# Performance work log

Measured on AMD Instinct MI355X. Metric: run time of the kernel, lower is better.

Reference implementation:

```python
import jax, jax.numpy as jnp
import numpy as np

B, T, D, H = 1, 2048, 1024, 16
HD = D // H
STRIDE = T // 256  # hierarchical global stride (T > 512 branch)


def _mha(q_in, k_in, v_in, Wqkv, bqkv, Wo, bo, nh):
    """torch nn.MultiheadAttention (batch_first, eval/no-dropout), returns (out, head-avg attn)."""
    b, tq, d = q_in.shape
    hd = d // nh
    Wq, Wk, Wv = jnp.split(Wqkv, 3, axis=0)
    bq, bk, bv = jnp.split(bqkv, 3)
    def heads(x, W, bb):
        return (x @ W.T + bb).reshape(b, x.shape[1], nh, hd).transpose(0, 2, 1, 3)
    q = heads(q_in, Wq, bq)
    k = heads(k_in, Wk, bk)
    v = heads(v_in, Wv, bv)
    scores = jnp.einsum('bhtd,bhsd->bhts', q, k) / np.float32(np.sqrt(hd))
    attn = jax.nn.softmax(scores, axis=-1)
    out = jnp.einsum('bhts,bhsd->bhtd', attn, v).transpose(0, 2, 1, 3).reshape(b, tq, d)
    return out @ Wo.T + bo, attn.mean(axis=1)


def _interp_linear(x, size):
    """F.interpolate(mode='linear', align_corners=False) along axis 1. x: [B, Ts, C]."""
    ts = x.shape[1]
    src = (jnp.arange(size, dtype=x.dtype) + 0.5) * (ts / size) - 0.5
    src = jnp.clip(src, 0.0, ts - 1)
    i0 = jnp.floor(src).astype(jnp.int32)
    i1 = jnp.minimum(i0 + 1, ts - 1)
    w = (src - i0.astype(x.dtype))[None, :, None]
    return x[:, i0, :] * (1.0 - w) + x[:, i1, :] * w


def setup_inputs() -> dict:
    rng = jax.random.key(0)
    ks = iter(jax.random.split(rng, 32))
    s = 0.02
    n = lambda shape: jax.random.normal(next(ks), shape, dtype=jnp.float32) * s
    return {
        'query': jax.random.normal(next(ks), (B, T, D), jnp.float32),
        'key': jax.random.normal(next(ks), (B, T, D), jnp.float32),
        'value': jax.random.normal(next(ks), (B, T, D), jnp.float32),
        'strategy_probs': jax.nn.softmax(jax.random.normal(next(ks), (B, 4), jnp.float32), -1),
        'Wqkv_lin': n((3 * D, D)), 'b_lin': jnp.zeros((3 * D,), jnp.float32),
        'Wo_lin': n((D, D)), 'bo_lin': jnp.zeros((D,), jnp.float32),
        'sparsity_pattern': jax.random.normal(next(ks), (H, 1, 1), jnp.float32),
        'Wqkv_loc': n((3 * D, D)), 'b_loc': jnp.zeros((3 * D,), jnp.float32),
        'Wo_loc': n((D, D)), 'bo_loc': jnp.zeros((D,), jnp.float32),
        'Wqkv_glb': n((3 * D, D)), 'b_glb': jnp.zeros((3 * D,), jnp.float32),
        'Wo_glb': n((D, D)), 'bo_glb': jnp.zeros((D,), jnp.float32),
        'Wf': n((D, 2 * D)), 'bf': jnp.zeros((D,), jnp.float32),
        'R_quant': jax.random.normal(next(ks), (H, HD, HD), jnp.float32),
        'ent_gate': jax.random.normal(next(ks), (H, 2, 2), jnp.float32),
    }


def reference(query, key, value, strategy_probs, Wqkv_lin, b_lin, Wo_lin, bo_lin,
              sparsity_pattern, Wqkv_loc, b_loc, Wo_loc, bo_loc,
              Wqkv_glb, b_glb, Wo_glb, bo_glb, Wf, bf, R_quant, ent_gate):
    b, t, d = query.shape
    hd = d // H
    scale = np.float32(np.sqrt(hd))
    # --- 1) "linear" branch: standard MHA ---
    linear_out, linear_w = _mha(query, key, value, Wqkv_lin, b_lin, Wo_lin, bo_lin, H)
    # --- 2) sparse branch (per-head learned on/off mask on raw scores) ---
    qh = query.reshape(b, t, H, hd).transpose(0, 2, 1, 3)
    kh = key.reshape(b, t, H, hd).transpose(0, 2, 1, 3)
    vh = value.reshape(b, t, H, hd).transpose(0, 2, 1, 3)
    scores = jnp.einsum('bhtd,bhsd->bhts', qh, kh) / scale
    mask = (jax.nn.sigmoid(sparsity_pattern) > 0.5).astype(scores.dtype)  # [H,1,1]
    sp_attn = jax.nn.softmax(scores * mask[None], axis=-1)
    sparse_out = jnp.einsum('bhts,bhsd->bhtd', sp_attn, vh).transpose(0, 2, 1, 3).reshape(b, t, d)
    sparse_w = sp_attn.mean(axis=1)
    # --- 3) hierarchical branch (T > 512 path: strided global + linear interp) ---
    local_out, _ = _mha(query, key, value, Wqkv_loc, b_loc, Wo_loc, bo_loc, H // 2)
    gq, gk, gv = query[:, ::STRIDE], key[:, ::STRIDE], value[:, ::STRIDE]
    g_small, _ = _mha(gq, gk, gv, Wqkv_glb, b_glb, Wo_glb, bo_glb, H // 2)
    global_out = _interp_linear(g_small, t)
    hier_out = jnp.concatenate([local_out, global_out], axis=-1) @ Wf.T + bf
    # --- 4) quantum branch (per-head rotation + scalar gate on scores) ---
    q_rot = jnp.einsum('bhtd,hde->bhte', qh, R_quant)
    k_rot = jnp.einsum('bhtd,hde->bhte', kh, R_quant)
    gate = jax.nn.sigmoid(ent_gate[:, 0, 0])[None, :, None, None]  # [1,H,1,1]
    q_attn = jax.nn.softmax((jnp.einsum('bhtd,bhsd->bhts', q_rot, k_rot) / scale) * gate, axis=-1)
    quantum_out = jnp.einsum('bhts,bhsd->bhtd', q_attn, vh).transpose(0, 2, 1, 3).reshape(b, t, d)
    quantum_w = q_attn.mean(axis=1)
    # --- blend via strategy probabilities ---
    sp = strategy_probs[:, :, None]  # [B,4,1]
    all_out = jnp.stack([linear_out, sparse_out, hier_out, quantum_out], axis=1)  # [B,4,T,D]
    weighted = (all_out * sp[..., None]).sum(axis=1)  # [B,T,D]
    wstack = jnp.stack([linear_w, sparse_w, quantum_w], axis=1)  # [B,3,T,T]
    wsel = sp[:, jnp.array([0, 1, 3])][..., None, None]  # [B,3,1,1,1] (faithful to source; requires B==1)
    combined = (wstack * wsel).sum(axis=1)
    return weighted, combined
```

## Files before the change

kernel.cpp:

```cpp
#include <hip/hip_runtime.h>
#include <math.h>

#define D_MODEL 1024

typedef __attribute__((ext_vector_type(8))) short bf16x8;
typedef __attribute__((ext_vector_type(4))) float f32x4;
typedef __attribute__((ext_vector_type(8))) unsigned short u16x8;

__device__ __forceinline__ unsigned short bfr(float f) {
    unsigned u = __float_as_uint(f);
    u += 0x7fffu + ((u >> 16) & 1u);
    return (unsigned short)(u >> 16);
}
__device__ __forceinline__ float bff(unsigned short s) {
    return __uint_as_float(((unsigned)s) << 16);
}
__device__ __forceinline__ void split2(float x, unsigned short &h, unsigned short &l) {
    h = bfr(x);
    l = bfr(x - bff(h));
}
__device__ __forceinline__ unsigned cvtpk(float a, float b) {
    unsigned r;
    asm("v_cvt_pk_bf16_f32 %0, %1, %2" : "=v"(r) : "v"(a), "v"(b));
    return r;
}
__device__ __forceinline__ f32x4 mfma3(bf16x8 ah, bf16x8 al, bf16x8 bh, bf16x8 bl, f32x4 c) {
    c = __builtin_amdgcn_mfma_f32_16x16x32_bf16(ah, bh, c, 0, 0, 0);
    c = __builtin_amdgcn_mfma_f32_16x16x32_bf16(ah, bl, c, 0, 0, 0);
    c = __builtin_amdgcn_mfma_f32_16x16x32_bf16(al, bh, c, 0, 0, 0);
    return c;
}

__global__ __launch_bounds__(256) void split_rm(
    const float* __restrict__ in, unsigned short* __restrict__ hi,
    unsigned short* __restrict__ lo, int n4)
{
    int idx = blockIdx.x * 256 + threadIdx.x;
    if (idx >= n4) return;
    float4 v = ((const float4*)in)[idx];
    ushort4 hs, ls;
    split2(v.x, hs.x, ls.x); split2(v.y, hs.y, ls.y);
    split2(v.z, hs.z, ls.z); split2(v.w, hs.w, ls.w);
    ((ushort4*)hi)[idx] = hs;
    ((ushort4*)lo)[idx] = ls;
}

__global__ __launch_bounds__(256) void split_tr(
    const float* __restrict__ in, unsigned short* __restrict__ hi,
    unsigned short* __restrict__ lo, int T)
{
    __shared__ float xs[64][65];
    const int t0 = blockIdx.x * 64, d0 = blockIdx.y * 64;
    for (int idx = threadIdx.x; idx < 64 * 16; idx += 256) {
        int r = idx >> 4, c4 = (idx & 15) * 4;
        float4 v = *(const float4*)&in[(size_t)(t0 + r) * D_MODEL + d0 + c4];
        xs[r][c4] = v.x; xs[r][c4 + 1] = v.y; xs[r][c4 + 2] = v.z; xs[r][c4 + 3] = v.w;
    }
    __syncthreads();
    for (int idx = threadIdx.x; idx < 64 * 8; idx += 256) {
        int dd = idx >> 3, t8 = (idx & 7) * 8;
        u16x8 hs, ls;
#pragma unroll
        for (int j = 0; j < 8; ++j) {
            unsigned short hh, ll;
            split2(xs[t8 + j][dd], hh, ll);
            hs[j] = hh; ls[j] = ll;
        }
        *(u16x8*)&hi[(size_t)(d0 + dd) * T + t0 + t8] = hs;
        *(u16x8*)&lo[(size_t)(d0 + dd) * T + t0 + t8] = ls;
    }
}

__global__ __launch_bounds__(256) void gemm_mfma(
    const float* __restrict__ X, int xrstride,
    const float* __restrict__ W, int wrstride,
    const float* __restrict__ bias,
    float* __restrict__ C, int M, int N, int K,
    const float* __restrict__ sptr, int sidx, int accum)
{
    __shared__ unsigned short Xh[64][40], Xl[64][40];
    __shared__ unsigned short Wh[64][40], Wl[64][40];
    const int tid = threadIdx.x;
    const int m0 = blockIdx.x * 64, n0 = blockIdx.y * 64;
    const int lane = tid & 63, wave = tid >> 6;
    const int c = lane & 15, quad = lane >> 4;
    const int mbase = wave * 16;

    f32x4 acc[4];
#pragma unroll
    for (int nt = 0; nt < 4; ++nt) acc[nt] = (f32x4){0.f, 0.f, 0.f, 0.f};

    float4 xr[2], wr[2];
    const int r_ = tid >> 3, d4_ = (tid & 7) * 4;
    const int r2_ = (tid + 256) >> 3, d42_ = ((tid + 256) & 7) * 4;
    auto ldXW = [&](int k0) {
        xr[0] = *(const float4*)&X[(size_t)(m0 + r_) * xrstride + k0 + d4_];
        xr[1] = *(const float4*)&X[(size_t)(m0 + r2_) * xrstride + k0 + d42_];
        wr[0] = *(const float4*)&W[(size_t)(n0 + r_) * wrstride + k0 + d4_];
        wr[1] = *(const float4*)&W[(size_t)(n0 + r2_) * wrstride + k0 + d42_];
    };
    ldXW(0);

    for (int k0 = 0; k0 < K; k0 += 32) {
        __syncthreads();
        {
            ushort4 hs, ls;
            split2(xr[0].x, hs.x, ls.x); split2(xr[0].y, hs.y, ls.y);
            split2(xr[0].z, hs.z, ls.z); split2(xr[0].w, hs.w, ls.w);
            *(ushort4*)&Xh[r_][d4_] = hs; *(ushort4*)&Xl[r_][d4_] = ls;
            split2(xr[1].x, hs.x, ls.x); split2(xr[1].y, hs.y, ls.y);
            split2(xr[1].z, hs.z, ls.z); split2(xr[1].w, hs.w, ls.w);
            *(ushort4*)&Xh[r2_][d42_] = hs; *(ushort4*)&Xl[r2_][d42_] = ls;
            split2(wr[0].x, hs.x, ls.x); split2(wr[0].y, hs.y, ls.y);
            split2(wr[0].z, hs.z, ls.z); split2(wr[0].w, hs.w, ls.w);
            *(ushort4*)&Wh[r_][d4_] = hs; *(ushort4*)&Wl[r_][d4_] = ls;
            split2(wr[1].x, hs.x, ls.x); split2(wr[1].y, hs.y, ls.y);
            split2(wr[1].z, hs.z, ls.z); split2(wr[1].w, hs.w, ls.w);
            *(ushort4*)&Wh[r2_][d42_] = hs; *(ushort4*)&Wl[r2_][d42_] = ls;
        }
        __syncthreads();
        if (k0 + 32 < K) ldXW(k0 + 32);
        bf16x8 ah = *(const bf16x8*)&Xh[mbase + c][quad * 8];
        bf16x8 al = *(const bf16x8*)&Xl[mbase + c][quad * 8];
#pragma unroll
        for (int nt = 0; nt < 4; ++nt) {
            bf16x8 bh = *(const bf16x8*)&Wh[nt * 16 + c][quad * 8];
            bf16x8 bl = *(const bf16x8*)&Wl[nt * 16 + c][quad * 8];
            acc[nt] = mfma3(ah, al, bh, bl, acc[nt]);
        }
    }
    const float s = (sptr != nullptr) ? sptr[sidx] : 1.0f;
#pragma unroll
    for (int nt = 0; nt < 4; ++nt) {
#pragma unroll
        for (int reg = 0; reg < 4; ++reg) {
            int row = m0 + mbase + quad * 4 + reg;
            int col = n0 + nt * 16 + c;
            float v = acc[nt][reg] + (bias ? bias[col] : 0.0f);
            v *= s;
            size_t gi = (size_t)row * N + col;
            if (accum) v += C[gi];
            C[gi] = v;
        }
    }
}

template <int HD>
__global__ __launch_bounds__(256) void flash_mfma(
    const float* __restrict__ Q,
    const unsigned short* __restrict__ Khi, const unsigned short* __restrict__ Klo,
    const unsigned short* __restrict__ Vthi, const unsigned short* __restrict__ Vtlo,
    const float* __restrict__ aparam, int amode,
    float* __restrict__ O, float* __restrict__ O2,
    const float* __restrict__ strat, int o_sidx, int accum,
    float* __restrict__ mout, float* __restrict__ lout,
    int Tq, int Tk, float inv_scale)
{
    constexpr int ROWS = 64;
    constexpr int STILE = (HD == 64) ? 64 : 32;
    constexpr int MT   = STILE / 16;
    constexpr int KS   = HD / 32;
    constexpr int NT_O = HD / 16;
    constexpr int KS_PV = STILE / 32;
    constexpr int QP = HD + 8;
    constexpr int SP = STILE + 8;
    constexpr int KIT = STILE * HD / 8 / 256;
    constexpr int VIT = STILE * HD / 8 / 256;

    __shared__ __align__(16) unsigned short Kh[STILE][QP], Kl[STILE][QP];
    __shared__ __align__(16) unsigned short Vh[HD][SP],  Vl[HD][SP];
    __shared__ __align__(16) unsigned short Ph[ROWS][SP], Pl[ROWS][SP];

    const int tid = threadIdx.x;
    const int h = blockIdx.y;
    const int r0 = blockIdx.x * ROWS;
    const int lane = tid & 63, wave = tid >> 6;
    const int c = lane & 15, quad = lane >> 4;
    const int mbase = wave * 16;
    const int ZS = gridDim.z;
    const int tkloc = Tk / ZS;
    const int kv0 = blockIdx.z * tkloc;

    float gate = 1.0f;
    if (amode == 1) gate = (aparam[h] > 0.0f) ? 1.0f : 0.0f;
    if (amode == 2) gate = 1.0f / (1.0f + __expf(-aparam[h * 4]));
    const float ascale = gate * inv_scale;
    const bool masked = (amode == 1) && (gate == 0.0f);

    bf16x8 qah[KS], qal[KS];
    if (!masked) {
        const float* qrow = &Q[(size_t)(r0 + mbase + c) * D_MODEL + h * HD];
#pragma unroll
        for (int ks = 0; ks < KS; ++ks) {
            float4 a  = *(const float4*)(qrow + ks * 32 + quad * 8);
            float4 b2 = *(const float4*)(qrow + ks * 32 + quad * 8 + 4);
            unsigned short hh, ll;
            split2(a.x, hh, ll);  qah[ks][0] = (short)hh; qal[ks][0] = (short)ll;
            split2(a.y, hh, ll);  qah[ks][1] = (short)hh; qal[ks][1] = (short)ll;
            split2(a.z, hh, ll);  qah[ks][2] = (short)hh; qal[ks][2] = (short)ll;
            split2(a.w, hh, ll);  qah[ks][3] = (short)hh; qal[ks][3] = (short)ll;
            split2(b2.x, hh, ll); qah[ks][4] = (short)hh; qal[ks][4] = (short)ll;
            split2(b2.y, hh, ll); qah[ks][5] = (short)hh; qal[ks][5] = (short)ll;
            split2(b2.z, hh, ll); qah[ks][6] = (short)hh; qal[ks][6] = (short)ll;
            split2(b2.w, hh, ll); qah[ks][7] = (short)hh; qal[ks][7] = (short)ll;
        }
    }

    float mreg = -1e30f, lacc = 0.0f;
    f32x4 oacc[NT_O];
#pragma unroll
    for (int nt = 0; nt < NT_O; ++nt) oacc[nt] = (f32x4){0.f, 0.f, 0.f, 0.f};

    bf16x8 pone, pzero;
#pragma unroll
    for (int j = 0; j < 8; ++j) { pone[j] = (short)0x3F80; pzero[j] = 0; }

    u16x8 krh[KIT], krl[KIT], vrh[VIT], vrl[VIT];

    auto load_regs = [&](int s0) {
        if (!masked) {
#pragma unroll
            for (int it = 0; it < KIT; ++it) {
                int idx = tid + it * 256;
                int r = idx / (HD / 8), c8 = (idx % (HD / 8)) * 8;
                size_t go = (size_t)(s0 + r) * D_MODEL + h * HD + c8;
                krh[it] = *(const u16x8*)&Khi[go];
                krl[it] = *(const u16x8*)&Klo[go];
            }
        }
#pragma unroll
        for (int it = 0; it < VIT; ++it) {
            int idx = tid + it * 256;
            int d = idx % HD, s8 = (idx / HD) * 8;
            size_t go = (size_t)(h * HD + d) * Tk + s0 + s8;
            vrh[it] = *(const u16x8*)&Vthi[go];
            vrl[it] = *(const u16x8*)&Vtlo[go];
        }
    };
    auto write_bufs = [&]() {
        if (!masked) {
#pragma unroll
            for (int it = 0; it < KIT; ++it) {
                int idx = tid + it * 256;
                int r = idx / (HD / 8), c8 = (idx % (HD / 8)) * 8;
                *(u16x8*)&Kh[r][c8] = krh[it];
                *(u16x8*)&Kl[r][c8] = krl[it];
            }
        }
#pragma unroll
        for (int it = 0; it < VIT; ++it) {
            int idx = tid + it * 256;
            int d = idx % HD, s8 = (idx / HD) * 8;
            *(u16x8*)&Vh[d][s8] = vrh[it];
            *(u16x8*)&Vl[d][s8] = vrl[it];
        }
    };

    auto compute_tile = [&]() {
        if (!masked) {
            f32x4 sf[MT];
#pragma unroll
            for (int mt = 0; mt < MT; ++mt) {
                f32x4 s = (f32x4){0.f, 0.f, 0.f, 0.f};
#pragma unroll
                for (int ks = 0; ks < KS; ++ks) {
                    bf16x8 kh = *(const bf16x8*)&Kh[mt * 16 + c][ks * 32 + quad * 8];
                    bf16x8 kl = *(const bf16x8*)&Kl[mt * 16 + c][ks * 32 + quad * 8];
                    s = mfma3(kh, kl, qah[ks], qal[ks], s);
                }
                sf[mt] = s * ascale;
            }
            float tm = sf[0][0];
#pragma unroll
            for (int mt = 0; mt < MT; ++mt)
#pragma unroll
                for (int reg = 0; reg < 4; ++reg) tm = fmaxf(tm, sf[mt][reg]);
            if (__any(tm > mreg + 8.0f)) {
                tm = fmaxf(tm, __shfl_xor(tm, 16));
                tm = fmaxf(tm, __shfl_xor(tm, 32));
                float nm = fmaxf(mreg, tm);
                float al = __expf(mreg - nm);
                mreg = nm;
                lacc *= al;
                float ar[4];
#pragma unroll
                for (int reg = 0; reg < 4; ++reg)
                    ar[reg] = __shfl(al, (lane & 48) | (quad * 4 + reg));
#pragma unroll
                for (int nt = 0; nt < NT_O; ++nt)
#pragma unroll
                    for (int reg = 0; reg < 4; ++reg) oacc[nt][reg] *= ar[reg];
            }
#pragma unroll
            for (int mt = 0; mt < MT; ++mt) {
                float p0 = __expf(sf[mt][0] - mreg);
                float p1 = __expf(sf[mt][1] - mreg);
                float p2 = __expf(sf[mt][2] - mreg);
                float p3 = __expf(sf[mt][3] - mreg);
                lacc += (p0 + p1) + (p2 + p3);
                unsigned h01 = cvtpk(p0, p1), h23 = cvtpk(p2, p3);
                float b0 = __uint_as_float(h01 << 16);
                float b1 = __uint_as_float(h01 & 0xffff0000u);
                float b2 = __uint_as_float(h23 << 16);
                float b3 = __uint_as_float(h23 & 0xffff0000u);
                unsigned l01 = cvtpk(p0 - b0, p1 - b1);
                unsigned l23 = cvtpk(p2 - b2, p3 - b3);
                uint2 hw; hw.x = h01; hw.y = h23;
                uint2 lw; lw.x = l01; lw.y = l23;
                *(uint2*)&Ph[mbase + c][mt * 16 + quad * 4] = hw;
                *(uint2*)&Pl[mbase + c][mt * 16 + quad * 4] = lw;
            }
        }
        bf16x8 pah[KS_PV], pal[KS_PV];
#pragma unroll
        for (int ks = 0; ks < KS_PV; ++ks) {
            if (masked) { pah[ks] = pone; pal[ks] = pzero; }
            else {
                pah[ks] = *(const bf16x8*)&Ph[mbase + c][ks * 32 + quad * 8];
                pal[ks] = *(const bf16x8*)&Pl[mbase + c][ks * 32 + quad * 8];
            }
        }
#pragma unroll
        for (int nt = 0; nt < NT_O; ++nt) {
            f32x4 o = oacc[nt];
#pragma unroll
            for (int ks = 0; ks < KS_PV; ++ks) {
                bf16x8 bh = *(const bf16x8*)&Vh[nt * 16 + c][ks * 32 + quad * 8];
                bf16x8 bl = *(const bf16x8*)&Vl[nt * 16 + c][ks * 32 + quad * 8];
                o = mfma3(pah[ks], pal[ks], bh, bl, o);
            }
            oacc[nt] = o;
        }
    };

    const int NTL = tkloc / STILE;
    load_regs(kv0);
    for (int t = 0; t < NTL; ++t) {
        __syncthreads();
        write_bufs();
        __syncthreads();
        if (t + 1 < NTL) load_regs(kv0 + (t + 1) * STILE);
        compute_tile();
    }

    lacc += __shfl_xor(lacc, 16);
    lacc += __shfl_xor(lacc, 32);

    if (ZS == 1) {
        const float osc = (o_sidx >= 0) ? strat[o_sidx] : 1.0f;
        if (quad == 0) {
            int row = r0 + mbase + c;
            mout[h * Tq + row] = masked ? 0.0f : mreg;
            lout[h * Tq + row] = masked ? (float)Tk : lacc;
        }
        float sc[4];
#pragma unroll
        for (int reg = 0; reg < 4; ++reg) {
            float lf = masked ? (float)Tk
                              : __shfl(lacc, (lane & 48) | (quad * 4 + reg));
            sc[reg] = osc / lf;
        }
#pragma unroll
        for (int reg = 0; reg < 4; ++reg) {
            int row = r0 + mbase + quad * 4 + reg;
#pragma unroll
            for (int nt = 0; nt < NT_O; ++nt) {
                size_t gi = (size_t)row * D_MODEL + h * HD + nt * 16 + c;
                float v = sc[reg] * oacc[nt][reg];
                if (accum) v += O[gi];
                O[gi] = v;
            }
        }
    } else {
        float* Op = (blockIdx.z == 0) ? O : O2;
        if (quad == 0) {
            int row = r0 + mbase + c;
            mout[(blockIdx.z * gridDim.y + h) * Tq + row] = masked ? 0.0f : mreg;
            lout[(blockIdx.z * gridDim.y + h) * Tq + row] = masked ? (float)tkloc : lacc;
        }
#pragma unroll
        for (int reg = 0; reg < 4; ++reg) {
            int row = r0 + mbase + quad * 4 + reg;
#pragma unroll
            for (int nt = 0; nt < NT_O; ++nt)
                Op[(size_t)row * D_MODEL + h * HD + nt * 16 + c] = oacc[nt][reg];
        }
    }
}

__global__ __launch_bounds__(256) void combine2(
    const float* __restrict__ O0, const float* __restrict__ O1,
    const float* __restrict__ mp, const float* __restrict__ lp,
    float* __restrict__ O, const float* __restrict__ strat,
    int o_sidx, int accum, int Tq)
{
    const int row = blockIdx.x;
    const int c4 = threadIdx.x * 4;
    const int h = c4 >> 7;
    const float m0 = mp[h * Tq + row], m1 = mp[(8 + h) * Tq + row];
    const float l0 = lp[h * Tq + row], l1 = lp[(8 + h) * Tq + row];
    const float m = fmaxf(m0, m1);
    const float w0 = __expf(m0 - m), w1 = __expf(m1 - m);
    const float osc = (o_sidx >= 0) ? strat[o_sidx] : 1.0f;
    const float sc = osc / (l0 * w0 + l1 * w1);
    float4 a = *(const float4*)&O0[(size_t)row * D_MODEL + c4];
    float4 b = *(const float4*)&O1[(size_t)row * D_MODEL + c4];
    size_t gi = (size_t)row * D_MODEL + c4;
    float4 r;
    r.x = sc * (a.x * w0 + b.x * w1);
    r.y = sc * (a.y * w0 + b.y * w1);
    r.z = sc * (a.z * w0 + b.z * w1);
    r.w = sc * (a.w * w0 + b.w * w1);
    if (accum) {
        float4 o = *(const float4*)&O[gi];
        r.x += o.x; r.y += o.y; r.z += o.z; r.w += o.w;
    }
    *(float4*)&O[gi] = r;
}

__global__ __launch_bounds__(256) void comb_mfma(
    const unsigned short* __restrict__ Qhi, const unsigned short* __restrict__ Qlo,
    const unsigned short* __restrict__ Khi, const unsigned short* __restrict__ Klo,
    const float* __restrict__ mrow, const float* __restrict__ lrow,
    const float* __restrict__ aparam, int amode,
    const float* __restrict__ strat,
    float* __restrict__ comb, int Tq, int Tk, int nh, float inv_scale)
{
    __shared__ __align__(16) unsigned short Kh[128][72], Kl[128][72];
    const int tid = threadIdx.x;
    const int r0 = blockIdx.x * 64, c0 = blockIdx.y * 128;
    const int lane = tid & 63, wave = tid >> 6;
    const int c = lane & 15, quad = lane >> 4;
    const int mbase = wave * 16;

    f32x4 acc[8];
#pragma unroll
    for (int nt = 0; nt < 8; ++nt) acc[nt] = (f32x4){0.f, 0.f, 0.f, 0.f};

    int hlist[16]; float glist[16]; int nact = 0; float unif = 0.0f;
    for (int h = 0; h < nh; ++h) {
        float gate = 1.0f;
        if (amode == 1) gate = (aparam[h] > 0.0f) ? 1.0f : 0.0f;
        if (amode == 2) gate = 1.0f / (1.0f + __expf(-aparam[h * 4]));
        if (amode == 1 && gate == 0.0f) { unif += 1.0f; continue; }
        hlist[nact] = h; glist[nact] = gate * inv_scale; ++nact;
    }

    u16x8 krh[4], krl[4];
    auto loadK = [&](int h) {
#pragma unroll
        for (int it = 0; it < 4; ++it) {
            int idx = tid + it * 256;
            int r = idx >> 3, c8 = (idx & 7) * 8;
            size_t go = (size_t)(c0 + r) * D_MODEL + h * 64 + c8;
            krh[it] = *(const u16x8*)&Khi[go];
            krl[it] = *(const u16x8*)&Klo[go];
        }
    };
    if (nact > 0) loadK(hlist[0]);

    for (int i = 0; i < nact; ++i) {
        const int h = hlist[i];
        const float ascale = glist[i];
        __syncthreads();
#pragma unroll
        for (int it = 0; it < 4; ++it) {
            int idx = tid + it * 256;
            int r = idx >> 3, c8 = (idx & 7) * 8;
            *(u16x8*)&Kh[r][c8] = krh[it];
            *(u16x8*)&Kl[r][c8] = krl[it];
        }
        __syncthreads();
        if (i + 1 < nact) loadK(hlist[i + 1]);

        bf16x8 qah[2], qal[2];
        const unsigned short* qh = &Qhi[(size_t)(r0 + mbase + c) * D_MODEL + h * 64];
        const unsigned short* ql = &Qlo[(size_t)(r0 + mbase + c) * D_MODEL + h * 64];
#pragma unroll
        for (int ks = 0; ks < 2; ++ks) {
            qah[ks] = *(const bf16x8*)(qh + ks * 32 + quad * 8);
            qal[ks] = *(const bf16x8*)(ql + ks * 32 + quad * 8);
        }

        float mr[4], li[4];
#pragma unroll
        for (int reg = 0; reg < 4; ++reg) {
            int row = r0 + mbase + quad * 4 + reg;
            mr[reg] = mrow[h * Tq + row];
            li[reg] = 1.0f / lrow[h * Tq + row];
        }
#pragma unroll
        for (int nt = 0; nt < 8; ++nt) {
            f32x4 s = (f32x4){0.f, 0.f, 0.f, 0.f};
#pragma unroll
            for (int ks = 0; ks < 2; ++ks) {
                bf16x8 bh = *(const bf16x8*)&Kh[nt * 16 + c][ks * 32 + quad * 8];
                bf16x8 bl = *(const bf16x8*)&Kl[nt * 16 + c][ks * 32 + quad * 8];
                s = mfma3(qah[ks], qal[ks], bh, bl, s);
            }
#pragma unroll
            for (int reg = 0; reg < 4; ++reg)
                acc[nt][reg] += __expf(s[reg] * ascale - mr[reg]) * li[reg];
        }
    }
    const float csc = (strat[0] + strat[1] + strat[3]) / (float)nh;
    const float uadd = unif / (float)Tk;
#pragma unroll
    for (int nt = 0; nt < 8; ++nt) {
#pragma unroll
        for (int reg = 0; reg < 4; ++reg) {
            int row = r0 + mbase + quad * 4 + reg;
            comb[(size_t)row * Tk + c0 + nt * 16 + c] = csc * (acc[nt][reg] + uadd);
        }
    }
}

__global__ __launch_bounds__(256) void rotate_heads(
    const float* __restrict__ X, const float* __restrict__ R,
    float* __restrict__ Y)
{
    __shared__ float Rt[64][68];
    __shared__ float xs[64][68];
    const int tid = threadIdx.x;
    const int h = blockIdx.y;
    const int t0 = blockIdx.x * 64;
    for (int idx = tid; idx < 4096; idx += 256) {
        int d = idx >> 6, e = idx & 63;
        Rt[e][d] = R[h * 4096 + idx];
        xs[d][e] = X[(size_t)(t0 + d) * D_MODEL + h * 64 + e];
    }
    __syncthreads();
    const int ty = tid >> 4, tx = tid & 15;
    float acc[4][4] = {};
#pragma unroll 4
    for (int d0 = 0; d0 < 64; d0 += 4) {
        float4 rv[4];
#pragma unroll
        for (int j = 0; j < 4; ++j) rv[j] = *(const float4*)&Rt[tx * 4 + j][d0];
#pragma unroll
        for (int i = 0; i < 4; ++i) {
            float4 a = *(const float4*)&xs[ty * 4 + i][d0];
#pragma unroll
            for (int j = 0; j < 4; ++j)
                acc[i][j] += a.x * rv[j].x + a.y * rv[j].y + a.z * rv[j].z + a.w * rv[j].w;
        }
    }
#pragma unroll
    for (int i = 0; i < 4; ++i)
#pragma unroll
        for (int j = 0; j < 4; ++j)
            Y[(size_t)(t0 + ty * 4 + i) * D_MODEL + h * 64 + tx * 4 + j] = acc[i][j];
}

__global__ __launch_bounds__(256) void interp_lin(
    const float* __restrict__ G, float* __restrict__ out)
{
    const int t = blockIdx.x;
    float src = (t + 0.5f) * 0.125f - 0.5f;
    src = fminf(fmaxf(src, 0.0f), 255.0f);
    float fl = floorf(src);
    int i0 = (int)fl;
    int i1 = min(i0 + 1, 255);
    float w = src - fl;
    const float4* g0 = (const float4*)(G + (size_t)i0 * D_MODEL);
    const float4* g1 = (const float4*)(G + (size_t)i1 * D_MODEL);
    float4* o = (float4*)(out + (size_t)t * D_MODEL);
    int c = threadIdx.x;
    float4 a = g0[c], b = g1[c];
    float4 r;
    r.x = a.x * (1.0f - w) + b.x * w;
    r.y = a.y * (1.0f - w) + b.y * w;
    r.z = a.z * (1.0f - w) + b.z * w;
    r.w = a.w * (1.0f - w) + b.w * w;
    o[c] = r;
}

extern "C" void kernel_launch(void* const* d_in, const int* in_sizes, int n_in,
                              void* d_out, int out_size, void* d_ws, size_t ws_size,
                              hipStream_t stream)
{
    (void)in_sizes; (void)n_in; (void)ws_size; (void)out_size;
    const float* query    = (const float*)d_in[0];
    const float* key      = (const float*)d_in[1];
    const float* value    = (const float*)d_in[2];
    const float* strat    = (const float*)d_in[3];
    const float* Wqkv_lin = (const float*)d_in[4];
    const float* b_lin    = (const float*)d_in[5];
    const float* Wo_lin   = (const float*)d_in[6];
    const float* bo_lin   = (const float*)d_in[7];
    const float* spars    = (const float*)d_in[8];
    const float* Wqkv_loc = (const float*)d_in[9];
    const float* b_loc    = (const float*)d_in[10];
    const float* Wo_loc   = (const float*)d_in[11];
    const float* bo_loc   = (const float*)d_in[12];
    const float* Wqkv_glb = (const float*)d_in[13];
    const float* b_glb    = (const float*)d_in[14];
    const float* Wo_glb   = (const float*)d_in[15];
    const float* bo_glb   = (const float*)d_in[16];
    const float* Wf       = (const float*)d_in[17];
    const float* bf       = (const float*)d_in[18];
    const float* Rq       = (const float*)d_in[19];
    const float* ent      = (const float*)d_in[20];

    float* out = (float*)d_out;
    float* weighted = out;
    float* combined = out + (size_t)2048 * 1024;
    const size_t PLANE = (size_t)2048 * 2048;

    float* ws   = (float*)d_ws;
    float* qkv  = ws;
    float* AO   = qkv + 6291456;
    float* LO   = AO + 2097152;
    float* gqkv = LO + 2097152;
    float* gAO  = gqkv + 786432;
    float* gOUT = gAO + 262144;
    float* GI   = gOUT + 262144;
    float* mb   = GI + 2097152;
    float* lb   = mb + 32768;
    float* qrot = qkv;
    float* krot = qkv + 2097152;
    unsigned short* Ksp_h = (unsigned short*)(lb + 32768);
    unsigned short* Ksp_l = Ksp_h + 2097152;
    unsigned short* Vtp_h = Ksp_l + 2097152;
    unsigned short* Vtp_l = Vtp_h + 2097152;
    unsigned short* gKs_h = Vtp_l + 2097152;
    unsigned short* gKs_l = gKs_h + 262144;
    unsigned short* gVt_h = gKs_l + 262144;
    unsigned short* gVt_l = gVt_h + 262144;
    unsigned short* Qsp_h = (unsigned short*)GI;
    unsigned short* Qsp_l = Qsp_h + 2097152;

    const float inv8   = 0.125f;
    const float inv128 = 1.0f / sqrtf(128.0f);
    const float* srcs[3] = {query, key, value};

    hipMemsetAsync(weighted, 0, (size_t)2097152 * sizeof(float), stream);

    for (int sl = 0; sl < 3; ++sl)
        gemm_mfma<<<dim3(32, 16), 256, 0, stream>>>(
            srcs[sl], 1024, Wqkv_lin + (size_t)sl * 1048576, 1024, b_lin + sl * 1024,
            qkv + (size_t)sl * 2097152, 2048, 1024, 1024, nullptr, 0, 0);
    split_rm<<<dim3(2048), 256, 0, stream>>>(qkv + 2097152, Ksp_h, Ksp_l, 524288);
    split_tr<<<dim3(32, 16), 256, 0, stream>>>(qkv + 4194304, Vtp_h, Vtp_l, 2048);
    flash_mfma<64><<<dim3(32, 16), 256, 0, stream>>>(
        qkv, Ksp_h, Ksp_l, Vtp_h, Vtp_l, nullptr, 0,
        AO, nullptr, strat, -1, 0, mb, lb, 2048, 2048, inv8);
    split_rm<<<dim3(2048), 256, 0, stream>>>(qkv, Qsp_h, Qsp_l, 524288);
    comb_mfma<<<dim3(32, 16), 256, 0, stream>>>(
        Qsp_h, Qsp_l, Ksp_h, Ksp_l, mb, lb, nullptr, 0, strat,
        combined + 0 * PLANE, 2048, 2048, 16, inv8);
    gemm_mfma<<<dim3(32, 16), 256, 0, stream>>>(
        AO, 1024, Wo_lin, 1024, bo_lin, weighted, 2048, 1024, 1024, strat, 0, 1);

    split_rm<<<dim3(2048), 256, 0, stream>>>(key, Ksp_h, Ksp_l, 524288);
    split_tr<<<dim3(32, 16), 256, 0, stream>>>(value, Vtp_h, Vtp_l, 2048);
    flash_mfma<64><<<dim3(32, 16), 256, 0, stream>>>(
        query, Ksp_h, Ksp_l, Vtp_h, Vtp_l, spars, 1,
        weighted, nullptr, strat, 1, 1, mb, lb, 2048, 2048, inv8);
    split_rm<<<dim3(2048), 256, 0, stream>>>(query, Qsp_h, Qsp_l, 524288);
    comb_mfma<<<dim3(32, 16), 256, 0, stream>>>(
        Qsp_h, Qsp_l, Ksp_h, Ksp_l, mb, lb, spars, 1, strat,
        combined + 1 * PLANE, 2048, 2048, 16, inv8);

    rotate_heads<<<dim3(32, 16), 256, 0, stream>>>(query, Rq, qrot);
    rotate_heads<<<dim3(32, 16), 256, 0, stream>>>(key, Rq, krot);
    split_rm<<<dim3(2048), 256, 0, stream>>>(krot, Ksp_h, Ksp_l, 524288);
    flash_mfma<64><<<dim3(32, 16), 256, 0, stream>>>(
        qrot, Ksp_h, Ksp_l, Vtp_h, Vtp_l, ent, 2,
        weighted, nullptr, strat, 3, 1, mb, lb, 2048, 2048, inv8);
    split_rm<<<dim3(2048), 256, 0, stream>>>(qrot, Qsp_h, Qsp_l, 524288);
    comb_mfma<<<dim3(32, 16), 256, 0, stream>>>(
        Qsp_h, Qsp_l, Ksp_h, Ksp_l, mb, lb, ent, 2, strat,
        combined + 2 * PLANE, 2048, 2048, 16, inv8);

    for (int sl = 0; sl < 3; ++sl)
        gemm_mfma<<<dim3(32, 16), 256, 0, stream>>>(
            srcs[sl], 1024, Wqkv_loc + (size_t)sl * 1048576, 1024, b_loc + sl * 1024,
            qkv + (size_t)sl * 2097152, 2048, 1024, 1024, nullptr, 0, 0);
    split_rm<<<dim3(2048), 256, 0, stream>>>(qkv + 2097152, Ksp_h, Ksp_l, 524288);
    split_tr<<<dim3(32, 16), 256, 0, stream>>>(qkv + 4194304, Vtp_h, Vtp_l, 2048);
    flash_mfma<128><<<dim3(32, 8, 2), 256, 0, stream>>>(
        qkv, Ksp_h, Ksp_l, Vtp_h, Vtp_l, nullptr, 0,
        AO, GI, strat, -1, 0, mb, lb, 2048, 2048, inv128);
    combine2<<<dim3(2048), 256, 0, stream>>>(
        AO, GI, mb, lb, AO, strat, -1, 0, 2048);
    gemm_mfma<<<dim3(32, 16), 256, 0, stream>>>(
        AO, 1024, Wo_loc, 1024, bo_loc, LO, 2048, 1024, 1024, nullptr, 0, 0);

    for (int sl = 0; sl < 3; ++sl)
        gemm_mfma<<<dim3(4, 16), 256, 0, stream>>>(
            srcs[sl], 8192, Wqkv_glb + (size_t)sl * 1048576, 1024, b_glb + sl * 1024,
            gqkv + (size_t)sl * 262144, 256, 1024, 1024, nullptr, 0, 0);
    split_rm<<<dim3(256), 256, 0, stream>>>(gqkv + 262144, gKs_h, gKs_l, 65536);
    split_tr<<<dim3(4, 16), 256, 0, stream>>>(gqkv + 524288, gVt_h, gVt_l, 256);
    flash_mfma<128><<<dim3(4, 8), 256, 0, stream>>>(
        gqkv, gKs_h, gKs_l, gVt_h, gVt_l, nullptr, 0,
        gAO, nullptr, strat, -1, 0, mb, lb, 256, 256, inv128);
    gemm_mfma<<<dim3(4, 16), 256, 0, stream>>>(
        gAO, 1024, Wo_glb, 1024, bo_glb, gOUT, 256, 1024, 1024, nullptr, 0, 0);
    interp_lin<<<dim3(2048), 256, 0, stream>>>(gOUT, GI);

    gemm_mfma<<<dim3(32, 16), 256, 0, stream>>>(
        LO, 1024, Wf, 2048, bf, weighted, 2048, 1024, 1024, strat, 2, 1);
    gemm_mfma<<<dim3(32, 16), 256, 0, stream>>>(
        GI, 1024, Wf + 1024, 2048, nullptr, weighted, 2048, 1024, 1024, strat, 2, 1);
}
```

Measured before the change: 1.253 ms.

## Batch QKV GEMMs over grid z, split-K flash for HD64, swizzle LDS, cache m/l

The three per-slice QKV projection GEMMs now run as one launch using blockIdx.z, and the two head rotations are merged into one launch the same way. The HD=64 flash attention passes now split the key range across two z-blocks, with a generalized combine kernel that merges the partials and writes the final row max and sum for the combined-weights kernel. LDS tiles for HD=64 use an XOR swizzle instead of padding to reduce bank conflicts. comb_mfma now stages per-row m and 1/l values in shared memory. These changes aim to cut launch count, raise occupancy on a small grid and lower LDS conflicts. In exchange they add an extra combine pass and a larger scratch buffer.

```diff
diff --git a/kernel.cpp b/kernel.cpp
--- a/kernel.cpp
+++ b/kernel.cpp
@@ -72,12 +72,19 @@
 }
 
 __global__ __launch_bounds__(256) void gemm_mfma(
-    const float* __restrict__ X, int xrstride,
-    const float* __restrict__ W, int wrstride,
-    const float* __restrict__ bias,
-    float* __restrict__ C, int M, int N, int K,
+    const float* __restrict__ X0, const float* __restrict__ X1,
+    const float* __restrict__ X2, int xrstride,
+    const float* __restrict__ W, size_t wz, int wrstride,
+    const float* __restrict__ bias, int bz,
+    float* __restrict__ C, size_t cz, int M, int N, int K,
     const float* __restrict__ sptr, int sidx, int accum)
 {
+    const int z = blockIdx.z;
+    const float* X = (z == 0) ? X0 : (z == 1 ? X1 : X2);
+    W += (size_t)z * wz;
+    if (bias) bias += z * bz;
+    C += (size_t)z * cz;
+
     __shared__ unsigned short Xh[64][40], Xl[64][40];
     __shared__ unsigned short Wh[64][40], Wl[64][40];
     const int tid = threadIdx.x;
@@ -162,14 +169,28 @@
     constexpr int KS   = HD / 32;
     constexpr int NT_O = HD / 16;
     constexpr int KS_PV = STILE / 32;
-    constexpr int QP = HD + 8;
-    constexpr int SP = STILE + 8;
+    constexpr bool SWZ = (HD == 64);
+    constexpr int KPITCH = SWZ ? HD : HD + 8;
+    constexpr int VPITCH = SWZ ? STILE : STILE + 8;
     constexpr int KIT = STILE * HD / 8 / 256;
     constexpr int VIT = STILE * HD / 8 / 256;
 
-    __shared__ __align__(16) unsigned short Kh[STILE][QP], Kl[STILE][QP];
-    __shared__ __align__(16) unsigned short Vh[HD][SP],  Vl[HD][SP];
-    __shared__ __align__(16) unsigned short Ph[ROWS][SP], Pl[ROWS][SP];
+    __shared__ __align__(16) unsigned short Kh[STILE * KPITCH], Kl[STILE * KPITCH];
+    __shared__ __align__(16) unsigned short Vh[HD * VPITCH],  Vl[HD * VPITCH];
+    __shared__ __align__(16) unsigned short Ph[ROWS * VPITCH], Pl[ROWS * VPITCH];
+
+    auto KIX = [](int r, int cc) {
+        return SWZ ? r * HD + ((cc & 7) | ((((cc >> 3) ^ r) & 7) << 3))
+                   : r * KPITCH + cc;
+    };
+    auto VIX = [](int d, int s) {
+        return SWZ ? d * STILE + ((s & 7) | ((((s >> 3) ^ d) & 7) << 3))
+                   : d * VPITCH + s;
+    };
+    auto PIX = [](int r, int cc) {
+        return SWZ ? r * STILE + ((cc & 7) | ((((cc >> 3) ^ r) & 7) << 3))
+                   : r * VPITCH + cc;
+    };
 
     const int tid = threadIdx.x;
     const int h = blockIdx.y;
@@ -243,16 +264,16 @@
             for (int it = 0; it < KIT; ++it) {
                 int idx = tid + it * 256;
                 int r = idx / (HD / 8), c8 = (idx % (HD / 8)) * 8;
-                *(u16x8*)&Kh[r][c8] = krh[it];
-                *(u16x8*)&Kl[r][c8] = krl[it];
+                *(u16x8*)&Kh[KIX(r, c8)] = krh[it];
+                *(u16x8*)&Kl[KIX(r, c8)] = krl[it];
             }
         }
 #pragma unroll
         for (int it = 0; it < VIT; ++it) {
             int idx = tid + it * 256;
             int d = idx % HD, s8 = (idx / HD) * 8;
-            *(u16x8*)&Vh[d][s8] = vrh[it];
-            *(u16x8*)&Vl[d][s8] = vrl[it];
+            *(u16x8*)&Vh[VIX(d, s8)] = vrh[it];
+            *(u16x8*)&Vl[VIX(d, s8)] = vrl[it];
         }
     };
 
@@ -264,8 +285,8 @@
                 f32x4 s = (f32x4){0.f, 0.f, 0.f, 0.f};
 #pragma unroll
                 for (int ks = 0; ks < KS; ++ks) {
-                    bf16x8 kh = *(const bf16x8*)&Kh[mt * 16 + c][ks * 32 + quad * 8];
-                    bf16x8 kl = *(const bf16x8*)&Kl[mt * 16 + c][ks * 32 + quad * 8];
+                    bf16x8 kh = *(const bf16x8*)&Kh[KIX(mt * 16 + c, ks * 32 + quad * 8)];
+                    bf16x8 kl = *(const bf16x8*)&Kl[KIX(mt * 16 + c, ks * 32 + quad * 8)];
                     s = mfma3(kh, kl, qah[ks], qal[ks], s);
                 }
                 sf[mt] = s * ascale;
@@ -307,8 +328,8 @@
                 unsigned l23 = cvtpk(p2 - b2, p3 - b3);
                 uint2 hw; hw.x = h01; hw.y = h23;
                 uint2 lw; lw.x = l01; lw.y = l23;
-                *(uint2*)&Ph[mbase + c][mt * 16 + quad * 4] = hw;
-                *(uint2*)&Pl[mbase + c][mt * 16 + quad * 4] = lw;
+                *(uint2*)&Ph[PIX(mbase + c, mt * 16 + quad * 4)] = hw;
+                *(uint2*)&Pl[PIX(mbase + c, mt * 16 + quad * 4)] = lw;
             }
         }
         bf16x8 pah[KS_PV], pal[KS_PV];
@@ -316,8 +337,8 @@
         for (int ks = 0; ks < KS_PV; ++ks) {
             if (masked) { pah[ks] = pone; pal[ks] = pzero; }
             else {
-                pah[ks] = *(const bf16x8*)&Ph[mbase + c][ks * 32 + quad * 8];
-                pal[ks] = *(const bf16x8*)&Pl[mbase + c][ks * 32 + quad * 8];
+                pah[ks] = *(const bf16x8*)&Ph[PIX(mbase + c, ks * 32 + quad * 8)];
+                pal[ks] = *(const bf16x8*)&Pl[PIX(mbase + c, ks * 32 + quad * 8)];
             }
         }
 #pragma unroll
@@ -325,8 +346,8 @@
             f32x4 o = oacc[nt];
 #pragma unroll
             for (int ks = 0; ks < KS_PV; ++ks) {
-                bf16x8 bh = *(const bf16x8*)&Vh[nt * 16 + c][ks * 32 + quad * 8];
-                bf16x8 bl = *(const bf16x8*)&Vl[nt * 16 + c][ks * 32 + quad * 8];
+                bf16x8 bh = *(const bf16x8*)&Vh[VIX(nt * 16 + c, ks * 32 + quad * 8)];
+                bf16x8 bl = *(const bf16x8*)&Vl[VIX(nt * 16 + c, ks * 32 + quad * 8)];
                 o = mfma3(pah[ks], pal[ks], bh, bl, o);
             }
             oacc[nt] = o;
@@ -388,21 +409,27 @@
     }
 }
 
-__global__ __launch_bounds__(256) void combine2(
+__global__ __launch_bounds__(256) void combineK(
     const float* __restrict__ O0, const float* __restrict__ O1,
     const float* __restrict__ mp, const float* __restrict__ lp,
-    float* __restrict__ O, const float* __restrict__ strat,
-    int o_sidx, int accum, int Tq)
+    float* __restrict__ O, float* __restrict__ mf, float* __restrict__ lf,
+    const float* __restrict__ strat, int o_sidx, int accum, int Tq,
+    int hdshift, int NH)
 {
     const int row = blockIdx.x;
     const int c4 = threadIdx.x * 4;
-    const int h = c4 >> 7;
-    const float m0 = mp[h * Tq + row], m1 = mp[(8 + h) * Tq + row];
-    const float l0 = lp[h * Tq + row], l1 = lp[(8 + h) * Tq + row];
+    const int h = c4 >> hdshift;
+    const float m0 = mp[h * Tq + row], m1 = mp[(NH + h) * Tq + row];
+    const float l0 = lp[h * Tq + row], l1 = lp[(NH + h) * Tq + row];
     const float m = fmaxf(m0, m1);
     const float w0 = __expf(m0 - m), w1 = __expf(m1 - m);
+    const float lsum = l0 * w0 + l1 * w1;
+    if (mf && (c4 & ((1 << hdshift) - 1)) == 0) {
+        mf[h * Tq + row] = m;
+        lf[h * Tq + row] = lsum;
+    }
     const float osc = (o_sidx >= 0) ? strat[o_sidx] : 1.0f;
-    const float sc = osc / (l0 * w0 + l1 * w1);
+    const float sc = osc / lsum;
     float4 a = *(const float4*)&O0[(size_t)row * D_MODEL + c4];
     float4 b = *(const float4*)&O1[(size_t)row * D_MODEL + c4];
     size_t gi = (size_t)row * D_MODEL + c4;
@@ -427,11 +454,18 @@
     float* __restrict__ comb, int Tq, int Tk, int nh, float inv_scale)
 {
     __shared__ __align__(16) unsigned short Kh[128][72], Kl[128][72];
+    __shared__ float msh[16 * 64], lsh[16 * 64];
     const int tid = threadIdx.x;
     const int r0 = blockIdx.x * 64, c0 = blockIdx.y * 128;
     const int lane = tid & 63, wave = tid >> 6;
     const int c = lane & 15, quad = lane >> 4;
     const int mbase = wave * 16;
+
+    for (int idx = tid; idx < nh * 64; idx += 256) {
+        int hh = idx >> 6, rr = idx & 63;
+        msh[idx] = mrow[hh * Tq + r0 + rr];
+        lsh[idx] = 1.0f / lrow[hh * Tq + r0 + rr];
+    }
 
     f32x4 acc[8];
 #pragma unroll
@@ -485,9 +519,8 @@
         float mr[4], li[4];
 #pragma unroll
         for (int reg = 0; reg < 4; ++reg) {
-            int row = r0 + mbase + quad * 4 + reg;
-            mr[reg] = mrow[h * Tq + row];
-            li[reg] = 1.0f / lrow[h * Tq + row];
+            mr[reg] = msh[h * 64 + mbase + quad * 4 + reg];
+            li[reg] = lsh[h * 64 + mbase + quad * 4 + reg];
         }
 #pragma unroll
         for (int nt = 0; nt < 8; ++nt) {
@@ -516,9 +549,12 @@
 }
 
 __global__ __launch_bounds__(256) void rotate_heads(
-    const float* __restrict__ X, const float* __restrict__ R,
-    float* __restrict__ Y)
-{
+    const float* __restrict__ X0, const float* __restrict__ X1,
+    const float* __restrict__ R,
+    float* __restrict__ Y0, float* __restrict__ Y1)
+{
+    const float* X = blockIdx.z ? X1 : X0;
+    float* Y = blockIdx.z ? Y1 : Y0;
     __shared__ float Rt[64][68];
     __shared__ float xs[64][68];
     const int tid = threadIdx.x;
@@ -616,10 +652,10 @@
     float* gOUT = gAO + 262144;
     float* GI   = gOUT + 262144;
     float* mb   = GI + 2097152;
-    float* lb   = mb + 32768;
+    float* lb   = mb + 65536;
     float* qrot = qkv;
     float* krot = qkv + 2097152;
-    unsigned short* Ksp_h = (unsigned short*)(lb + 32768);
+    unsigned short* Ksp_h = (unsigned short*)(lb + 65536);
     unsigned short* Ksp_l = Ksp_h + 2097152;
     unsigned short* Vtp_h = Ksp_l + 2097152;
     unsigned short* Vtp_l = Vtp_h + 2097152;
@@ -627,81 +663,89 @@
     unsigned short* gKs_l = gKs_h + 262144;
     unsigned short* gVt_h = gKs_l + 262144;
     unsigned short* gVt_l = gVt_h + 262144;
+    float* mc = (float*)(gVt_l + 262144);
+    float* lc = mc + 32768;
     unsigned short* Qsp_h = (unsigned short*)GI;
     unsigned short* Qsp_l = Qsp_h + 2097152;
 
     const float inv8   = 0.125f;
     const float inv128 = 1.0f / sqrtf(128.0f);
-    const float* srcs[3] = {query, key, value};
 
     hipMemsetAsync(weighted, 0, (size_t)2097152 * sizeof(float), stream);
 
-    for (int sl = 0; sl < 3; ++sl)
-        gemm_mfma<<<dim3(32, 16), 256, 0, stream>>>(
-            srcs[sl], 1024, Wqkv_lin + (size_t)sl * 1048576, 1024, b_lin + sl * 1024,
-            qkv + (size_t)sl * 2097152, 2048, 1024, 1024, nullptr, 0, 0);
+    gemm_mfma<<<dim3(32, 16, 3), 256, 0, stream>>>(
+        query, key, value, 1024, Wqkv_lin, 1048576, 1024, b_lin, 1024,
+        qkv, 2097152, 2048, 1024, 1024, nullptr, 0, 0);
     split_rm<<<dim3(2048), 256, 0, stream>>>(qkv + 2097152, Ksp_h, Ksp_l, 524288);
     split_tr<<<dim3(32, 16), 256, 0, stream>>>(qkv + 4194304, Vtp_h, Vtp_l, 2048);
-    flash_mfma<64><<<dim3(32, 16), 256, 0, stream>>>(
+    flash_mfma<64><<<dim3(32, 16, 2), 256, 0, stream>>>(
         qkv, Ksp_h, Ksp_l, Vtp_h, Vtp_l, nullptr, 0,
-        AO, nullptr, strat, -1, 0, mb, lb, 2048, 2048, inv8);
+        AO, GI, strat, -1, 0, mb, lb, 2048, 2048, inv8);
+    combineK<<<dim3(2048), 256, 0, stream>>>(
+        AO, GI, mb, lb, AO, mc, lc, strat, -1, 0, 2048, 6, 16);
     split_rm<<<dim3(2048), 256, 0, stream>>>(qkv, Qsp_h, Qsp_l, 524288);
     comb_mfma<<<dim3(32, 16), 256, 0, stream>>>(
-        Qsp_h, Qsp_l, Ksp_h, Ksp_l, mb, lb, nullptr, 0, strat,
+        Qsp_h, Qsp_l, Ksp_h, Ksp_l, mc, lc, nullptr, 0, strat,
         combined + 0 * PLANE, 2048, 2048, 16, inv8);
-    gemm_mfma<<<dim3(32, 16), 256, 0, stream>>>(
-        AO, 1024, Wo_lin, 1024, bo_lin, weighted, 2048, 1024, 1024, strat, 0, 1);
+    gemm_mfma<<<dim3(32, 16, 1), 256, 0, stream>>>(
+        AO, AO, AO, 1024, Wo_lin, 0, 1024, bo_lin, 0,
+        weighted, 0, 2048, 1024, 1024, strat, 0, 1);
 
     split_rm<<<dim3(2048), 256, 0, stream>>>(key, Ksp_h, Ksp_l, 524288);
     split_tr<<<dim3(32, 16), 256, 0, stream>>>(value, Vtp_h, Vtp_l, 2048);
-    flash_mfma<64><<<dim3(32, 16), 256, 0, stream>>>(
+    flash_mfma<64><<<dim3(32, 16, 2), 256, 0, stream>>>(
         query, Ksp_h, Ksp_l, Vtp_h, Vtp_l, spars, 1,
-        weighted, nullptr, strat, 1, 1, mb, lb, 2048, 2048, inv8);
+        AO, GI, strat, 1, 1, mb, lb, 2048, 2048, inv8);
+    combineK<<<dim3(2048), 256, 0, stream>>>(
+        AO, GI, mb, lb, weighted, mc, lc, strat, 1, 1, 2048, 6, 16);
     split_rm<<<dim3(2048), 256, 0, stream>>>(query, Qsp_h, Qsp_l, 524288);
     comb_mfma<<<dim3(32, 16), 256, 0, stream>>>(
-        Qsp_h, Qsp_l, Ksp_h, Ksp_l, mb, lb, spars, 1, strat,
+        Qsp_h, Qsp_l, Ksp_h, Ksp_l, mc, lc, spars, 1, strat,
         combined + 1 * PLANE, 2048, 2048, 16, inv8);
 
-    rotate_heads<<<dim3(32, 16), 256, 0, stream>>>(query, Rq, qrot);
-    rotate_heads<<<dim3(32, 16), 256, 0, stream>>>(key, Rq, krot);
+    rotate_heads<<<dim3(32, 16, 2), 256, 0, stream>>>(query, key, Rq, qrot, krot);
     split_rm<<<dim3(2048), 256, 0, stream>>>(krot, Ksp_h, Ksp_l, 524288);
-    flash_mfma<64><<<dim3(32, 16), 256, 0, stream>>>(
+    flash_mfma<64><<<dim3(32, 16, 2), 256, 0, stream>>>(
         qrot, Ksp_h, Ksp_l, Vtp_h, Vtp_l, ent, 2,
-        weighted, nullptr, strat, 3, 1, mb, lb, 2048, 2048, inv8);
+        AO, GI, strat, 3, 1, mb, lb, 2048, 2048, inv8);
+    combineK<<<dim3(2048), 256, 0, stream>>>(
+        AO, GI, mb, lb, weighted, mc, lc, strat, 3, 1, 2048, 6, 16);
     split_rm<<<dim3(2048), 256, 0, stream>>>(qrot, Qsp_h, Qsp_l, 524288);
     comb_mfma<<<dim3(32, 16), 256, 0, stream>>>(
-        Qsp_h, Qsp_l, Ksp_h, Ksp_l, mb, lb, ent, 2, strat,
+        Qsp_h, Qsp_l, Ksp_h, Ksp_l, mc, lc, ent, 2, strat,
         combined + 2 * PLANE, 2048, 2048, 16, inv8);
 
-    for (int sl = 0; sl < 3; ++sl)
-        gemm_mfma<<<dim3(32, 16), 256, 0, stream>>>(
-            srcs[sl], 1024, Wqkv_loc + (size_t)sl * 1048576, 1024, b_loc + sl * 1024,
-            qkv + (size_t)sl * 2097152, 2048, 1024, 1024, nullptr, 0, 0);
+    gemm_mfma<<<dim3(32, 16, 3), 256, 0, stream>>>(
+        query, key, value, 1024, Wqkv_loc, 1048576, 1024, b_loc, 1024,
+        qkv, 2097152, 2048, 1024, 1024, nullptr, 0, 0);
     split_rm<<<dim3(2048), 256, 0, stream>>>(qkv + 2097152, Ksp_h, Ksp_l, 524288);
     split_tr<<<dim3(32, 16), 256, 0, stream>>>(qkv + 4194304, Vtp_h, Vtp_l, 2048);
     flash_mfma<128><<<dim3(32, 8, 2), 256, 0, stream>>>(
         qkv, Ksp_h, Ksp_l, Vtp_h, Vtp_l, nullptr, 0,
         AO, GI, strat, -1, 0, mb, lb, 2048, 2048, inv128);
-    combine2<<<dim3(2048), 256, 0, stream>>>(
-        AO, GI, mb, lb, AO, strat, -1, 0, 2048);
-    gemm_mfma<<<dim3(32, 16), 256, 0, stream>>>(
-        AO, 1024, Wo_loc, 1024, bo_loc, LO, 2048, 1024, 1024, nullptr, 0, 0);
-
-    for (int sl = 0; sl < 3; ++sl)
-        gemm_mfma<<<dim3(4, 16), 256, 0, stream>>>(
-            srcs[sl], 8192, Wqkv_glb + (size_t)sl * 1048576, 1024, b_glb + sl * 1024,
-            gqkv + (size_t)sl * 262144, 256, 1024, 1024, nullptr, 0, 0);
+    combineK<<<dim3(2048), 256, 0, stream>>>(
+        AO, GI, mb, lb, AO, nullptr, nullptr, strat, -1, 0, 2048, 7, 8);
+    gemm_mfma<<<dim3(32, 16, 1), 256, 0, stream>>>(
+        AO, AO, AO, 1024, Wo_loc, 0, 1024, bo_loc, 0,
+        LO, 0, 2048, 1024, 1024, nullptr, 0, 0);
+
+    gemm_mfma<<<dim3(4, 16, 3), 256, 0, stream>>>(
+        query, key, value, 8192, Wqkv_glb, 1048576, 1024, b_glb, 1024,
+        gqkv, 262144, 256, 1024, 1024, nullptr, 0, 0);
     split_rm<<<dim3(256), 256, 0, stream>>>(gqkv + 262144, gKs_h, gKs_l, 65536);
     split_tr<<<dim3(4, 16), 256, 0, stream>>>(gqkv + 524288, gVt_h, gVt_l, 256);
-    flash_mfma<128><<<dim3(4, 8), 256, 0, stream>>>(
+    flash_mfma<128><<<dim3(4, 8, 1), 256, 0, stream>>>(
         gqkv, gKs_h, gKs_l, gVt_h, gVt_l, nullptr, 0,
         gAO, nullptr, strat, -1, 0, mb, lb, 256, 256, inv128);
-    gemm_mfma<<<dim3(4, 16), 256, 0, stream>>>(
-        gAO, 1024, Wo_glb, 1024, bo_glb, gOUT, 256, 1024, 1024, nullptr, 0, 0);
+    gemm_mfma<<<dim3(4, 16, 1), 256, 0, stream>>>(
+        gAO, gAO, gAO, 1024, Wo_glb, 0, 1024, bo_glb, 0,
+        gOUT, 0, 256, 1024, 1024, nullptr, 0, 0);
     interp_lin<<<dim3(2048), 256, 0, stream>>>(gOUT, GI);
 
-    gemm_mfma<<<dim3(32, 16), 256, 0, stream>>>(
-        LO, 1024, Wf, 2048, bf, weighted, 2048, 1024, 1024, strat, 2, 1);
-    gemm_mfma<<<dim3(32, 16), 256, 0, stream>>>(
-        GI, 1024, Wf + 1024, 2048, nullptr, weighted, 2048, 1024, 1024, strat, 2, 1);
-}
+    gemm_mfma<<<dim3(32, 16, 1), 256, 0, stream>>>(
+        LO, LO, LO, 1024, Wf, 0, 2048, bf, 0,
+        weighted, 0, 2048, 1024, 1024, strat, 2, 1);
+    gemm_mfma<<<dim3(32, 16, 1), 256, 0, stream>>>(
+        GI, GI, GI, 1024, Wf + 1024, 0, 2048, nullptr, 0,
+        weighted, 0, 2048, 1024, 1024, strat, 2, 1);
+}
```

Measured after the change: 1.078 ms. 1.16x faster.
